# Kernel optimization log

Hardware: AMD Instinct MI355X
Metric: run time of the kernel (lower is better)

The kernel has to match this reference:

```python
import jax, jax.numpy as jnp
import numpy as np

HID = 128
NH = 4
HD = HID // NH
SCALE = HD ** -0.5
EPS = 1e-8


def setup_inputs() -> dict:
    key = jax.random.key(0)
    ks = jax.random.split(key, 10)
    C, S, H = 4, 4096, HID
    x = jax.random.normal(ks[0], (C, S, H), dtype=jnp.float32)
    edge_weight = jax.random.uniform(ks[1], (C, S, S), dtype=jnp.float32)
    def lin(kw, kb):
        W = jax.random.normal(kw, (H, H), dtype=jnp.float32) * (1.0 / np.sqrt(H))
        b = jax.random.normal(kb, (H,), dtype=jnp.float32) * 0.01
        return W, b
    Wq, bq = lin(ks[2], ks[3])
    Wk, bk = lin(ks[4], ks[5])
    Wv, bv = lin(ks[6], ks[7])
    Wo, bo = lin(ks[8], ks[9])
    return {"x": x, "edge_weight": edge_weight,
            "Wq": Wq, "bq": bq, "Wk": Wk, "bk": bk,
            "Wv": Wv, "bv": bv, "Wo": Wo, "bo": bo}


def reference(x, edge_weight, Wq, bq, Wk, bk, Wv, bv, Wo, bo):
    C, S, H = x.shape
    # projections (torch Linear: x @ W.T + b), split into heads -> (C, nh, S, hd)
    def proj(W, b):
        return (x @ W.T + b).reshape(C, S, NH, HD).transpose(0, 2, 1, 3)
    q = proj(Wq, bq)
    k = proj(Wk, bk)
    v = proj(Wv, bv)
    # scores with additive log structure bias: (C, nh, S, S)
    scores = jnp.einsum('chqd,chkd->chqk', q, k) * SCALE
    scores = scores + jnp.log(jnp.maximum(edge_weight, EPS))[:, None, :, :]
    attn = jax.nn.softmax(scores, axis=-1)  # dropout is identity in eval
    out = jnp.einsum('chqk,chkd->chqd', attn, v)
    out = out.transpose(0, 2, 1, 3).reshape(C, S, H)
    return out @ Wo.T + bo
```

## Files before the change

### kernel.cpp

```cpp
#include <hip/hip_runtime.h>
#include <hip/hip_bf16.h>
#include <cstdint>

#define S_LEN 4096
#define NHEAD 4
#define HDIM 32
#define HID 128
#define CBATCH 4
#define EPSW 1e-8f
#define NCHUNKS (S_LEN / 32)

typedef __attribute__((ext_vector_type(8))) short short8v;
typedef __attribute__((ext_vector_type(4))) float float4v;

__device__ __forceinline__ unsigned short f2bf(float f) {
    unsigned int u = __float_as_uint(f);
    return (unsigned short)((u + 0x7fffu + ((u >> 16) & 1u)) >> 16);
}

__device__ __forceinline__ float exp2_asm(float x) {
    float r;
    asm("v_exp_f32 %0, %1" : "=v"(r) : "v"(x));
    return r;
}

__device__ __forceinline__ unsigned cvt_pk_bf16(float lo, float hi) {
    unsigned r;
    asm("v_cvt_pk_bf16_f32 %0, %1, %2" : "=v"(r) : "v"(lo), "v"(hi));
    return r;
}

__device__ __forceinline__ void gload16(const void* g, void* l) {
    __builtin_amdgcn_global_load_lds(
        (const __attribute__((address_space(1))) void*)g,
        (__attribute__((address_space(3))) void*)l,
        16, 0, 0);
}

__global__ __launch_bounds__(256) void qkv_proj_kernel(
    const float* __restrict__ x,
    const float* __restrict__ Wq, const float* __restrict__ bq,
    const float* __restrict__ Wk, const float* __restrict__ bk,
    const float* __restrict__ Wv, const float* __restrict__ bv,
    unsigned short* __restrict__ Qo, unsigned short* __restrict__ Ko,
    unsigned short* __restrict__ Vo)
{
    __shared__ float xs[64][132];
    __shared__ float wsT[64][68];

    const int tid = threadIdx.x;
    const int mrow0 = blockIdx.x * 64;
    const int n0 = blockIdx.y * 64;
    const int p = blockIdx.z;
    const float* W    = (p == 0) ? Wq : (p == 1) ? Wk : Wv;
    const float* bias = (p == 0) ? bq : (p == 1) ? bk : bv;
    unsigned short* Out = (p == 0) ? Qo : (p == 1) ? Ko : Vo;

    for (int i = tid; i < 64 * 32; i += 256) {
        int r = i >> 5, c4 = (i & 31) * 4;
        *(float4*)&xs[r][c4] = *(const float4*)&x[(size_t)(mrow0 + r) * HID + c4];
    }

    float acc[4][4] = {};
    const int tr = tid >> 4;
    const int tc = tid & 15;

    for (int ph = 0; ph < 2; ++ph) {
        __syncthreads();
        for (int i = tid; i < 64 * 16; i += 256) {
            int r = i >> 4, c4 = (i & 15) * 4;
            float4 wv = *(const float4*)&W[(size_t)(n0 + r) * HID + ph * 64 + c4];
            wsT[c4 + 0][r] = wv.x;
            wsT[c4 + 1][r] = wv.y;
            wsT[c4 + 2][r] = wv.z;
            wsT[c4 + 3][r] = wv.w;
        }
        __syncthreads();
        #pragma unroll 4
        for (int k4 = 0; k4 < 16; ++k4) {
            float4 xv[4];
            #pragma unroll
            for (int i = 0; i < 4; ++i)
                xv[i] = *(const float4*)&xs[tr * 4 + i][ph * 64 + k4 * 4];
            #pragma unroll
            for (int kk = 0; kk < 4; ++kk) {
                float4 wv = *(const float4*)&wsT[k4 * 4 + kk][tc * 4];
                #pragma unroll
                for (int i = 0; i < 4; ++i) {
                    float xk = ((const float*)&xv[i])[kk];
                    acc[i][0] += xk * wv.x;
                    acc[i][1] += xk * wv.y;
                    acc[i][2] += xk * wv.z;
                    acc[i][3] += xk * wv.w;
                }
            }
        }
    }

    const float scale = (p == 0) ? 0.25500544458521289f : 1.0f;
    float4 bv4 = *(const float4*)&bias[n0 + tc * 4];
    const int nbase = n0 + tc * 4;
    const int h = nbase >> 5;
    const int d = nbase & 31;
    #pragma unroll
    for (int i = 0; i < 4; ++i) {
        int m = mrow0 + tr * 4 + i;
        int c = m >> 12, s = m & 4095;
        unsigned short pk[4];
        pk[0] = f2bf((acc[i][0] + bv4.x) * scale);
        pk[1] = f2bf((acc[i][1] + bv4.y) * scale);
        pk[2] = f2bf((acc[i][2] + bv4.z) * scale);
        pk[3] = f2bf((acc[i][3] + bv4.w) * scale);
        *(uint2*)&Out[((size_t)(c * NHEAD + h) * S_LEN + s) * HDIM + d] = *(uint2*)pk;
    }
}

__global__ __launch_bounds__(256) void vtrans_kernel(
    const unsigned short* __restrict__ V, unsigned short* __restrict__ Vt2)
{
    __shared__ unsigned short vs[64][40];
    const int tid = threadIdx.x;
    const int chh = blockIdx.y;
    const int s0 = blockIdx.x * 64;
    const size_t base = (size_t)chh * S_LEN * HDIM;
    {
        int r = tid >> 2, ch = (tid & 3) * 8;
        *(uint4*)&vs[r][ch] = *(const uint4*)&V[base + (size_t)(s0 + r) * HDIM + ch];
    }
    __syncthreads();
    {
        const int lchunk = tid >> 7;
        const int db = (tid >> 6) & 1;
        const int l = tid & 63;
        const int li = l & 15;
        const int g = l >> 4;
        unsigned short pk[8];
        #pragma unroll
        for (int j = 0; j < 8; ++j) {
            int key = lchunk * 32 + ((j < 4) ? (4 * g + j) : (16 + 4 * g + (j - 4)));
            pk[j] = vs[key][db * 16 + li];
        }
        size_t chunk = (size_t)(s0 >> 5) + lchunk;
        *(uint4*)&Vt2[(((size_t)chh * 2 + db) * NCHUNKS + chunk) * 512 + l * 8] = *(uint4*)pk;
    }
}

template<int NS>
__global__ __launch_bounds__(256) void attn_kernel(
    const unsigned short* __restrict__ Q, const unsigned short* __restrict__ K,
    const unsigned short* __restrict__ Vt2, const float* __restrict__ ew,
    unsigned short* __restrict__ partO, float* __restrict__ den)
{
    const int KCHUNK = S_LEN / NS;
    const int NIT = KCHUNK / 32;

    __shared__ float ew_lds[3][1024];

    const int tid = threadIdx.x;
    const int w = tid >> 6;
    const int lane = tid & 63;
    const int li = lane & 15;
    const int g = lane >> 4;
    const int c = blockIdx.y;
    const int qbase = blockIdx.x * 32;
    const int split = blockIdx.z;
    const int kb0 = split * KCHUNK;
    const int chh = c * NHEAD + w;

    const size_t hb = (size_t)chh * S_LEN * HDIM;
    const unsigned short* Qh = Q + hb;
    const unsigned short* Kh = K + hb;
    const float* ewc = ew + (size_t)c * S_LEN * S_LEN;

    short8v qf0 = *(const short8v*)&Qh[(size_t)(qbase + li) * HDIM + g * 8];
    short8v qf1 = *(const short8v*)&Qh[(size_t)(qbase + 16 + li) * HDIM + g * 8];

    const float* ew_src = ewc + (size_t)(qbase + (w >> 1) * 16 + li) * S_LEN + kb0
                        + (w & 1) * 16 + g * 4;
    const unsigned short* kp  = Kh + (size_t)(kb0 + li) * HDIM + g * 8;
    const unsigned short* vp0 = Vt2 + (((size_t)chh * 2 + 0) * NCHUNKS + (kb0 >> 5)) * 512 + lane * 8;
    const unsigned short* vp1 = Vt2 + (((size_t)chh * 2 + 1) * NCHUNKS + (kb0 >> 5)) * 512 + lane * 8;

    float4v o00 = {}, o01 = {}, o10 = {}, o11 = {};
    float den0 = 0.f, den1 = 0.f;
    const float4v zero4 = {0.f, 0.f, 0.f, 0.f};

    #define CFENCE() asm volatile("" ::: "memory")

    short8v kf0 = *(const short8v*)kp;
    short8v kf1 = *(const short8v*)(kp + 512);
    short8v vf0 = *(const short8v*)vp0;
    short8v vf1 = *(const short8v*)vp1;
    CFENCE();
    gload16(ew_src,      &ew_lds[0][w * 256]);
    gload16(ew_src + 32, &ew_lds[1][w * 256]);
    ew_src += 64;
    CFENCE();

    int bew = 0;
    int sew = 2;
    for (int it = 0; it < NIT; ++it) {
        if (it > 0) {
            CFENCE();
            __builtin_amdgcn_s_barrier();
        }
        short8v nkf0, nkf1, nvf0, nvf1;
        if (it + 1 < NIT) {
            nkf0 = *(const short8v*)(kp + 1024);
            nkf1 = *(const short8v*)(kp + 1536);
            nvf0 = *(const short8v*)(vp0 + 512);
            nvf1 = *(const short8v*)(vp1 + 512);
        }
        CFENCE();
        if (it + 2 < NIT) {
            gload16(ew_src, &ew_lds[sew][w * 256]);
            ew_src += 32;
        }
        if (it == 0)               asm volatile("s_waitcnt vmcnt(6)" ::: "memory");
        else if (it + 2 < NIT)     asm volatile("s_waitcnt vmcnt(10)" ::: "memory");
        else if (it + 1 < NIT)     asm volatile("s_waitcnt vmcnt(9)" ::: "memory");
        else                       asm volatile("s_waitcnt vmcnt(4)" ::: "memory");
        __builtin_amdgcn_s_barrier();
        CFENCE();

        const float* eb = ew_lds[bew];
        float4 e00 = *(const float4*)&eb[lane * 4];
        float4 e01 = *(const float4*)&eb[256 + lane * 4];
        float4 e10 = *(const float4*)&eb[512 + lane * 4];
        float4 e11 = *(const float4*)&eb[768 + lane * 4];

        float4v s0 = __builtin_amdgcn_mfma_f32_16x16x32_bf16(kf0, qf0, zero4, 0, 0, 0);
        float4v s1 = __builtin_amdgcn_mfma_f32_16x16x32_bf16(kf1, qf0, zero4, 0, 0, 0);
        float4v s2 = __builtin_amdgcn_mfma_f32_16x16x32_bf16(kf0, qf1, zero4, 0, 0, 0);
        float4v s3 = __builtin_amdgcn_mfma_f32_16x16x32_bf16(kf1, qf1, zero4, 0, 0, 0);

        float p0 = fmaxf(e00.x, EPSW) * exp2_asm(s0[0]);
        float p1 = fmaxf(e00.y, EPSW) * exp2_asm(s0[1]);
        float p2 = fmaxf(e00.z, EPSW) * exp2_asm(s0[2]);
        float p3 = fmaxf(e00.w, EPSW) * exp2_asm(s0[3]);
        float p4 = fmaxf(e01.x, EPSW) * exp2_asm(s1[0]);
        float p5 = fmaxf(e01.y, EPSW) * exp2_asm(s1[1]);
        float p6 = fmaxf(e01.z, EPSW) * exp2_asm(s1[2]);
        float p7 = fmaxf(e01.w, EPSW) * exp2_asm(s1[3]);
        union { short8v v; unsigned u[4]; } pu0;
        pu0.u[0] = cvt_pk_bf16(p0, p1);
        pu0.u[1] = cvt_pk_bf16(p2, p3);
        pu0.u[2] = cvt_pk_bf16(p4, p5);
        pu0.u[3] = cvt_pk_bf16(p6, p7);
        den0 += ((p0 + p1) + (p2 + p3)) + ((p4 + p5) + (p6 + p7));
        o00 = __builtin_amdgcn_mfma_f32_16x16x32_bf16(vf0, pu0.v, o00, 0, 0, 0);
        o01 = __builtin_amdgcn_mfma_f32_16x16x32_bf16(vf1, pu0.v, o01, 0, 0, 0);

        float r0 = fmaxf(e10.x, EPSW) * exp2_asm(s2[0]);
        float r1 = fmaxf(e10.y, EPSW) * exp2_asm(s2[1]);
        float r2 = fmaxf(e10.z, EPSW) * exp2_asm(s2[2]);
        float r3 = fmaxf(e10.w, EPSW) * exp2_asm(s2[3]);
        float r4 = fmaxf(e11.x, EPSW) * exp2_asm(s3[0]);
        float r5 = fmaxf(e11.y, EPSW) * exp2_asm(s3[1]);
        float r6 = fmaxf(e11.z, EPSW) * exp2_asm(s3[2]);
        float r7 = fmaxf(e11.w, EPSW) * exp2_asm(s3[3]);
        union { short8v v; unsigned u[4]; } pu1;
        pu1.u[0] = cvt_pk_bf16(r0, r1);
        pu1.u[1] = cvt_pk_bf16(r2, r3);
        pu1.u[2] = cvt_pk_bf16(r4, r5);
        pu1.u[3] = cvt_pk_bf16(r6, r7);
        den1 += ((r0 + r1) + (r2 + r3)) + ((r4 + r5) + (r6 + r7));
        o10 = __builtin_amdgcn_mfma_f32_16x16x32_bf16(vf0, pu1.v, o10, 0, 0, 0);
        o11 = __builtin_amdgcn_mfma_f32_16x16x32_bf16(vf1, pu1.v, o11, 0, 0, 0);

        if (it + 1 < NIT) {
            kf0 = nkf0; kf1 = nkf1; vf0 = nvf0; vf1 = nvf1;
            kp += 1024; vp0 += 512; vp1 += 512;
        }
        bew = (bew == 2) ? 0 : bew + 1;
        sew = (sew == 2) ? 0 : sew + 1;
    }
    #undef CFENCE

    den0 += __shfl_xor(den0, 16, 64);
    den0 += __shfl_xor(den0, 32, 64);
    den1 += __shfl_xor(den1, 16, 64);
    den1 += __shfl_xor(den1, 32, 64);

    const size_t pbase = (((size_t)split * CBATCH + c) * NHEAD + w) * S_LEN + qbase;
    {
        const size_t pb = pbase + li;
        uint2 s;
        s.x = cvt_pk_bf16(o00[0], o00[1]);
        s.y = cvt_pk_bf16(o00[2], o00[3]);
        *(uint2*)&partO[pb * HDIM + 0 * 16 + g * 4] = s;
        s.x = cvt_pk_bf16(o01[0], o01[1]);
        s.y = cvt_pk_bf16(o01[2], o01[3]);
        *(uint2*)&partO[pb * HDIM + 1 * 16 + g * 4] = s;
        if (g == 0) den[pb] = den0;
    }
    {
        const size_t pb = pbase + 16 + li;
        uint2 s;
        s.x = cvt_pk_bf16(o10[0], o10[1]);
        s.y = cvt_pk_bf16(o10[2], o10[3]);
        *(uint2*)&partO[pb * HDIM + 0 * 16 + g * 4] = s;
        s.x = cvt_pk_bf16(o11[0], o11[1]);
        s.y = cvt_pk_bf16(o11[2], o11[3]);
        *(uint2*)&partO[pb * HDIM + 1 * 16 + g * 4] = s;
        if (g == 0) den[pb] = den1;
    }
}

template<int NS>
__global__ __launch_bounds__(256) void combine_kernel(
    const unsigned short* __restrict__ pO, const float* __restrict__ den,
    float* __restrict__ attnbuf)
{
    const int idx = blockIdx.x * 256 + threadIdx.x;
    const int d4 = idx & 7;
    const int q  = (idx >> 3) & (S_LEN - 1);
    const int h  = (idx >> 15) & 3;
    const int c  = idx >> 17;

    const size_t bq = ((size_t)c * NHEAD + h) * S_LEN + q;
    const size_t plane = (size_t)CBATCH * NHEAD * S_LEN;
    float4 acc = {0.f, 0.f, 0.f, 0.f};
    float dsum = 0.f;
    #pragma unroll
    for (int s = 0; s < NS; ++s) {
        const size_t b = (size_t)s * plane + bq;
        uint2 a = *(const uint2*)&pO[b * HDIM + d4 * 4];
        acc.x += __uint_as_float(a.x << 16);
        acc.y += __uint_as_float(a.x & 0xffff0000u);
        acc.z += __uint_as_float(a.y << 16);
        acc.w += __uint_as_float(a.y & 0xffff0000u);
        dsum += den[b];
    }
    float inv = 1.0f / dsum;
    float4 o;
    o.x = acc.x * inv;
    o.y = acc.y * inv;
    o.z = acc.z * inv;
    o.w = acc.w * inv;
    *(float4*)&attnbuf[((size_t)c * S_LEN + q) * HID + h * HDIM + d4 * 4] = o;
}

__global__ __launch_bounds__(256) void out_proj_kernel(
    const float* __restrict__ ain, const float* __restrict__ Wo,
    const float* __restrict__ bo, float* __restrict__ out)
{
    __shared__ float xs[64][132];
    __shared__ float wsT[64][68];

    const int tid = threadIdx.x;
    const int mrow0 = blockIdx.x * 64;
    const int n0 = blockIdx.y * 64;

    for (int i = tid; i < 64 * 32; i += 256) {
        int r = i >> 5, c4 = (i & 31) * 4;
        *(float4*)&xs[r][c4] = *(const float4*)&ain[(size_t)(mrow0 + r) * HID + c4];
    }

    float acc[4][4] = {};
    const int tr = tid >> 4;
    const int tc = tid & 15;

    for (int ph = 0; ph < 2; ++ph) {
        __syncthreads();
        for (int i = tid; i < 64 * 16; i += 256) {
            int r = i >> 4, c4 = (i & 15) * 4;
            float4 wv = *(const float4*)&Wo[(size_t)(n0 + r) * HID + ph * 64 + c4];
            wsT[c4 + 0][r] = wv.x;
            wsT[c4 + 1][r] = wv.y;
            wsT[c4 + 2][r] = wv.z;
            wsT[c4 + 3][r] = wv.w;
        }
        __syncthreads();
        #pragma unroll 4
        for (int k4 = 0; k4 < 16; ++k4) {
            float4 xv[4];
            #pragma unroll
            for (int i = 0; i < 4; ++i)
                xv[i] = *(const float4*)&xs[tr * 4 + i][ph * 64 + k4 * 4];
            #pragma unroll
            for (int kk = 0; kk < 4; ++kk) {
                float4 wv = *(const float4*)&wsT[k4 * 4 + kk][tc * 4];
                #pragma unroll
                for (int i = 0; i < 4; ++i) {
                    float xk = ((const float*)&xv[i])[kk];
                    acc[i][0] += xk * wv.x;
                    acc[i][1] += xk * wv.y;
                    acc[i][2] += xk * wv.z;
                    acc[i][3] += xk * wv.w;
                }
            }
        }
    }

    float4 bv4 = *(const float4*)&bo[n0 + tc * 4];
    #pragma unroll
    for (int i = 0; i < 4; ++i) {
        int m = mrow0 + tr * 4 + i;
        float4 o;
        o.x = acc[i][0] + bv4.x;
        o.y = acc[i][1] + bv4.y;
        o.z = acc[i][2] + bv4.z;
        o.w = acc[i][3] + bv4.w;
        *(float4*)&out[(size_t)m * HID + n0 + tc * 4] = o;
    }
}

extern "C" void kernel_launch(void* const* d_in, const int* in_sizes, int n_in,
                              void* d_out, int out_size, void* d_ws, size_t ws_size,
                              hipStream_t stream) {
    const float* x  = (const float*)d_in[0];
    const float* ew = (const float*)d_in[1];
    const float* Wq = (const float*)d_in[2];
    const float* bq = (const float*)d_in[3];
    const float* Wk = (const float*)d_in[4];
    const float* bk = (const float*)d_in[5];
    const float* Wv = (const float*)d_in[6];
    const float* bv = (const float*)d_in[7];
    const float* Wo = (const float*)d_in[8];
    const float* bo = (const float*)d_in[9];
    float* out = (float*)d_out;

    char* ws = (char*)d_ws;
    const size_t QSZ = (size_t)CBATCH * NHEAD * S_LEN * HDIM * sizeof(unsigned short);
    const size_t PLANE_O16 = (size_t)CBATCH * NHEAD * S_LEN * HDIM * sizeof(unsigned short);
    const size_t PLANE_D = (size_t)CBATCH * NHEAD * S_LEN * sizeof(float);

    const size_t need4 = 3 * QSZ + 4 * PLANE_O16 + 4 * PLANE_D;
    const int ns = (ws_size >= need4) ? 4 : 2;

    unsigned short* Qw  = (unsigned short*)(ws);
    unsigned short* Kw  = (unsigned short*)(ws + QSZ);
    unsigned short* Vt2 = (unsigned short*)(ws + 2 * QSZ);
    unsigned short* Vw  = (unsigned short*)(ws + 3 * QSZ);
    unsigned short* partO = (unsigned short*)(ws + 3 * QSZ);
    float* den   = (float*)(ws + 3 * QSZ + (size_t)ns * PLANE_O16);
    float* attnbuf = (float*)(ws);

    qkv_proj_kernel<<<dim3(256, 2, 3), 256, 0, stream>>>(x, Wq, bq, Wk, bk, Wv, bv, Qw, Kw, Vw);
    vtrans_kernel<<<dim3(S_LEN / 64, CBATCH * NHEAD), 256, 0, stream>>>(Vw, Vt2);
    if (ns == 4) {
        attn_kernel<4><<<dim3(S_LEN / 32, CBATCH, 4), 256, 0, stream>>>(Qw, Kw, Vt2, ew, partO, den);
        combine_kernel<4><<<dim3((CBATCH * S_LEN * HID / 4) / 256), 256, 0, stream>>>(partO, den, attnbuf);
    } else {
        attn_kernel<2><<<dim3(S_LEN / 32, CBATCH, 2), 256, 0, stream>>>(Qw, Kw, Vt2, ew, partO, den);
        combine_kernel<2><<<dim3((CBATCH * S_LEN * HID / 4) / 256), 256, 0, stream>>>(partO, den, attnbuf);
    }
    out_proj_kernel<<<dim3(256, 2), 256, 0, stream>>>(attnbuf, Wo, bo, out);
}
```

Baseline: 174.4 us.

## Process 64 keys per attention iteration with one barrier per step

The attention main loop now handles two 32-key sub-tiles per iteration, so the iteration count is halved. Each iteration stages a 2048-float edge-weight tile in a triple-buffered LDS ring with a prefetch distance of one, and drops the extra leading barrier. K/V fragments for both sub-tiles are loaded at the top of the same iteration instead of being prefetched into registers one iteration ahead. The aim is to cut barrier and loop overhead and give more independent MFMA/exp work per step. The cost is that K/V load latency may be less hidden, and LDS use doubles to 24 KB per block, which could lower occupancy.

```diff
diff --git a/kernel.cpp b/kernel.cpp
--- a/kernel.cpp
+++ b/kernel.cpp
@@ -152,9 +152,9 @@
     unsigned short* __restrict__ partO, float* __restrict__ den)
 {
     const int KCHUNK = S_LEN / NS;
-    const int NIT = KCHUNK / 32;
-
-    __shared__ float ew_lds[3][1024];
+    const int NIT = KCHUNK / 64;
+
+    __shared__ float ew_lds[3][2048];
 
     const int tid = threadIdx.x;
     const int w = tid >> 6;
@@ -175,8 +175,9 @@
     short8v qf0 = *(const short8v*)&Qh[(size_t)(qbase + li) * HDIM + g * 8];
     short8v qf1 = *(const short8v*)&Qh[(size_t)(qbase + 16 + li) * HDIM + g * 8];
 
-    const float* ew_src = ewc + (size_t)(qbase + (w >> 1) * 16 + li) * S_LEN + kb0
-                        + (w & 1) * 16 + g * 4;
+    const float* ewA_src = ewc + (size_t)(qbase + (w >> 1) * 16 + li) * S_LEN + kb0
+                         + (w & 1) * 16 + g * 4;
+    const float* ewB_src = ewA_src + 32;
     const unsigned short* kp  = Kh + (size_t)(kb0 + li) * HDIM + g * 8;
     const unsigned short* vp0 = Vt2 + (((size_t)chh * 2 + 0) * NCHUNKS + (kb0 >> 5)) * 512 + lane * 8;
     const unsigned short* vp1 = Vt2 + (((size_t)chh * 2 + 1) * NCHUNKS + (kb0 >> 5)) * 512 + lane * 8;
@@ -187,91 +188,130 @@
 
     #define CFENCE() asm volatile("" ::: "memory")
 
-    short8v kf0 = *(const short8v*)kp;
-    short8v kf1 = *(const short8v*)(kp + 512);
-    short8v vf0 = *(const short8v*)vp0;
-    short8v vf1 = *(const short8v*)vp1;
+    gload16(ewA_src, &ew_lds[0][w * 256]);
+    gload16(ewB_src, &ew_lds[0][1024 + w * 256]);
+    ewA_src += 64; ewB_src += 64;
     CFENCE();
-    gload16(ew_src,      &ew_lds[0][w * 256]);
-    gload16(ew_src + 32, &ew_lds[1][w * 256]);
-    ew_src += 64;
-    CFENCE();
 
     int bew = 0;
-    int sew = 2;
+    int sew = 1;
     for (int it = 0; it < NIT; ++it) {
-        if (it > 0) {
-            CFENCE();
-            __builtin_amdgcn_s_barrier();
-        }
-        short8v nkf0, nkf1, nvf0, nvf1;
+        short8v kfA0 = *(const short8v*)kp;
+        short8v kfA1 = *(const short8v*)(kp + 512);
+        short8v vfA0 = *(const short8v*)vp0;
+        short8v vfA1 = *(const short8v*)vp1;
+        short8v kfB0 = *(const short8v*)(kp + 1024);
+        short8v kfB1 = *(const short8v*)(kp + 1536);
+        short8v vfB0 = *(const short8v*)(vp0 + 512);
+        short8v vfB1 = *(const short8v*)(vp1 + 512);
+        CFENCE();
         if (it + 1 < NIT) {
-            nkf0 = *(const short8v*)(kp + 1024);
-            nkf1 = *(const short8v*)(kp + 1536);
-            nvf0 = *(const short8v*)(vp0 + 512);
-            nvf1 = *(const short8v*)(vp1 + 512);
-        }
-        CFENCE();
-        if (it + 2 < NIT) {
-            gload16(ew_src, &ew_lds[sew][w * 256]);
-            ew_src += 32;
-        }
-        if (it == 0)               asm volatile("s_waitcnt vmcnt(6)" ::: "memory");
-        else if (it + 2 < NIT)     asm volatile("s_waitcnt vmcnt(10)" ::: "memory");
-        else if (it + 1 < NIT)     asm volatile("s_waitcnt vmcnt(9)" ::: "memory");
-        else                       asm volatile("s_waitcnt vmcnt(4)" ::: "memory");
+            gload16(ewA_src, &ew_lds[sew][w * 256]);
+            gload16(ewB_src, &ew_lds[sew][1024 + w * 256]);
+            ewA_src += 64; ewB_src += 64;
+        }
+        if (it + 1 < NIT) asm volatile("s_waitcnt vmcnt(10)" ::: "memory");
+        else              asm volatile("s_waitcnt vmcnt(8)" ::: "memory");
         __builtin_amdgcn_s_barrier();
         CFENCE();
 
         const float* eb = ew_lds[bew];
-        float4 e00 = *(const float4*)&eb[lane * 4];
-        float4 e01 = *(const float4*)&eb[256 + lane * 4];
-        float4 e10 = *(const float4*)&eb[512 + lane * 4];
-        float4 e11 = *(const float4*)&eb[768 + lane * 4];
-
-        float4v s0 = __builtin_amdgcn_mfma_f32_16x16x32_bf16(kf0, qf0, zero4, 0, 0, 0);
-        float4v s1 = __builtin_amdgcn_mfma_f32_16x16x32_bf16(kf1, qf0, zero4, 0, 0, 0);
-        float4v s2 = __builtin_amdgcn_mfma_f32_16x16x32_bf16(kf0, qf1, zero4, 0, 0, 0);
-        float4v s3 = __builtin_amdgcn_mfma_f32_16x16x32_bf16(kf1, qf1, zero4, 0, 0, 0);
-
-        float p0 = fmaxf(e00.x, EPSW) * exp2_asm(s0[0]);
-        float p1 = fmaxf(e00.y, EPSW) * exp2_asm(s0[1]);
-        float p2 = fmaxf(e00.z, EPSW) * exp2_asm(s0[2]);
-        float p3 = fmaxf(e00.w, EPSW) * exp2_asm(s0[3]);
-        float p4 = fmaxf(e01.x, EPSW) * exp2_asm(s1[0]);
-        float p5 = fmaxf(e01.y, EPSW) * exp2_asm(s1[1]);
-        float p6 = fmaxf(e01.z, EPSW) * exp2_asm(s1[2]);
-        float p7 = fmaxf(e01.w, EPSW) * exp2_asm(s1[3]);
-        union { short8v v; unsigned u[4]; } pu0;
-        pu0.u[0] = cvt_pk_bf16(p0, p1);
-        pu0.u[1] = cvt_pk_bf16(p2, p3);
-        pu0.u[2] = cvt_pk_bf16(p4, p5);
-        pu0.u[3] = cvt_pk_bf16(p6, p7);
-        den0 += ((p0 + p1) + (p2 + p3)) + ((p4 + p5) + (p6 + p7));
-        o00 = __builtin_amdgcn_mfma_f32_16x16x32_bf16(vf0, pu0.v, o00, 0, 0, 0);
-        o01 = __builtin_amdgcn_mfma_f32_16x16x32_bf16(vf1, pu0.v, o01, 0, 0, 0);
-
-        float r0 = fmaxf(e10.x, EPSW) * exp2_asm(s2[0]);
-        float r1 = fmaxf(e10.y, EPSW) * exp2_asm(s2[1]);
-        float r2 = fmaxf(e10.z, EPSW) * exp2_asm(s2[2]);
-        float r3 = fmaxf(e10.w, EPSW) * exp2_asm(s2[3]);
-        float r4 = fmaxf(e11.x, EPSW) * exp2_asm(s3[0]);
-        float r5 = fmaxf(e11.y, EPSW) * exp2_asm(s3[1]);
-        float r6 = fmaxf(e11.z, EPSW) * exp2_asm(s3[2]);
-        float r7 = fmaxf(e11.w, EPSW) * exp2_asm(s3[3]);
-        union { short8v v; unsigned u[4]; } pu1;
-        pu1.u[0] = cvt_pk_bf16(r0, r1);
-        pu1.u[1] = cvt_pk_bf16(r2, r3);
-        pu1.u[2] = cvt_pk_bf16(r4, r5);
-        pu1.u[3] = cvt_pk_bf16(r6, r7);
-        den1 += ((r0 + r1) + (r2 + r3)) + ((r4 + r5) + (r6 + r7));
-        o10 = __builtin_amdgcn_mfma_f32_16x16x32_bf16(vf0, pu1.v, o10, 0, 0, 0);
-        o11 = __builtin_amdgcn_mfma_f32_16x16x32_bf16(vf1, pu1.v, o11, 0, 0, 0);
-
-        if (it + 1 < NIT) {
-            kf0 = nkf0; kf1 = nkf1; vf0 = nvf0; vf1 = nvf1;
-            kp += 1024; vp0 += 512; vp1 += 512;
-        }
+
+        {
+            float4 e00 = *(const float4*)&eb[lane * 4];
+            float4 e01 = *(const float4*)&eb[256 + lane * 4];
+            float4 e10 = *(const float4*)&eb[512 + lane * 4];
+            float4 e11 = *(const float4*)&eb[768 + lane * 4];
+
+            float4v s0 = __builtin_amdgcn_mfma_f32_16x16x32_bf16(kfA0, qf0, zero4, 0, 0, 0);
+            float4v s1 = __builtin_amdgcn_mfma_f32_16x16x32_bf16(kfA1, qf0, zero4, 0, 0, 0);
+            float4v s2 = __builtin_amdgcn_mfma_f32_16x16x32_bf16(kfA0, qf1, zero4, 0, 0, 0);
+            float4v s3 = __builtin_amdgcn_mfma_f32_16x16x32_bf16(kfA1, qf1, zero4, 0, 0, 0);
+
+            float p0 = fmaxf(e00.x, EPSW) * exp2_asm(s0[0]);
+            float p1 = fmaxf(e00.y, EPSW) * exp2_asm(s0[1]);
+            float p2 = fmaxf(e00.z, EPSW) * exp2_asm(s0[2]);
+            float p3 = fmaxf(e00.w, EPSW) * exp2_asm(s0[3]);
+            float p4 = fmaxf(e01.x, EPSW) * exp2_asm(s1[0]);
+            float p5 = fmaxf(e01.y, EPSW) * exp2_asm(s1[1]);
+            float p6 = fmaxf(e01.z, EPSW) * exp2_asm(s1[2]);
+            float p7 = fmaxf(e01.w, EPSW) * exp2_asm(s1[3]);
+            union { short8v v; unsigned u[4]; } pu0;
+            pu0.u[0] = cvt_pk_bf16(p0, p1);
+            pu0.u[1] = cvt_pk_bf16(p2, p3);
+            pu0.u[2] = cvt_pk_bf16(p4, p5);
+            pu0.u[3] = cvt_pk_bf16(p6, p7);
+            den0 += ((p0 + p1) + (p2 + p3)) + ((p4 + p5) + (p6 + p7));
+            o00 = __builtin_amdgcn_mfma_f32_16x16x32_bf16(vfA0, pu0.v, o00, 0, 0, 0);
+            o01 = __builtin_amdgcn_mfma_f32_16x16x32_bf16(vfA1, pu0.v, o01, 0, 0, 0);
+
+            float r0 = fmaxf(e10.x, EPSW) * exp2_asm(s2[0]);
+            float r1 = fmaxf(e10.y, EPSW) * exp2_asm(s2[1]);
+            float r2 = fmaxf(e10.z, EPSW) * exp2_asm(s2[2]);
+            float r3 = fmaxf(e10.w, EPSW) * exp2_asm(s2[3]);
+            float r4 = fmaxf(e11.x, EPSW) * exp2_asm(s3[0]);
+            float r5 = fmaxf(e11.y, EPSW) * exp2_asm(s3[1]);
+            float r6 = fmaxf(e11.z, EPSW) * exp2_asm(s3[2]);
+            float r7 = fmaxf(e11.w, EPSW) * exp2_asm(s3[3]);
+            union { short8v v; unsigned u[4]; } pu1;
+            pu1.u[0] = cvt_pk_bf16(r0, r1);
+            pu1.u[1] = cvt_pk_bf16(r2, r3);
+            pu1.u[2] = cvt_pk_bf16(r4, r5);
+            pu1.u[3] = cvt_pk_bf16(r6, r7);
+            den1 += ((r0 + r1) + (r2 + r3)) + ((r4 + r5) + (r6 + r7));
+            o10 = __builtin_amdgcn_mfma_f32_16x16x32_bf16(vfA0, pu1.v, o10, 0, 0, 0);
+            o11 = __builtin_amdgcn_mfma_f32_16x16x32_bf16(vfA1, pu1.v, o11, 0, 0, 0);
+        }
+
+        {
+            float4 e00 = *(const float4*)&eb[1024 + lane * 4];
+            float4 e01 = *(const float4*)&eb[1280 + lane * 4];
+            float4 e10 = *(const float4*)&eb[1536 + lane * 4];
+            float4 e11 = *(const float4*)&eb[1792 + lane * 4];
+
+            float4v s0 = __builtin_amdgcn_mfma_f32_16x16x32_bf16(kfB0, qf0, zero4, 0, 0, 0);
+            float4v s1 = __builtin_amdgcn_mfma_f32_16x16x32_bf16(kfB1, qf0, zero4, 0, 0, 0);
+            float4v s2 = __builtin_amdgcn_mfma_f32_16x16x32_bf16(kfB0, qf1, zero4, 0, 0, 0);
+            float4v s3 = __builtin_amdgcn_mfma_f32_16x16x32_bf16(kfB1, qf1, zero4, 0, 0, 0);
+
+            float p0 = fmaxf(e00.x, EPSW) * exp2_asm(s0[0]);
+            float p1 = fmaxf(e00.y, EPSW) * exp2_asm(s0[1]);
+            float p2 = fmaxf(e00.z, EPSW) * exp2_asm(s0[2]);
+            float p3 = fmaxf(e00.w, EPSW) * exp2_asm(s0[3]);
+            float p4 = fmaxf(e01.x, EPSW) * exp2_asm(s1[0]);
+            float p5 = fmaxf(e01.y, EPSW) * exp2_asm(s1[1]);
+            float p6 = fmaxf(e01.z, EPSW) * exp2_asm(s1[2]);
+            float p7 = fmaxf(e01.w, EPSW) * exp2_asm(s1[3]);
+            union { short8v v; unsigned u[4]; } pu0;
+            pu0.u[0] = cvt_pk_bf16(p0, p1);
+            pu0.u[1] = cvt_pk_bf16(p2, p3);
+            pu0.u[2] = cvt_pk_bf16(p4, p5);
+            pu0.u[3] = cvt_pk_bf16(p6, p7);
+            den0 += ((p0 + p1) + (p2 + p3)) + ((p4 + p5) + (p6 + p7));
+            o00 = __builtin_amdgcn_mfma_f32_16x16x32_bf16(vfB0, pu0.v, o00, 0, 0, 0);
+            o01 = __builtin_amdgcn_mfma_f32_16x16x32_bf16(vfB1, pu0.v, o01, 0, 0, 0);
+
+            float r0 = fmaxf(e10.x, EPSW) * exp2_asm(s2[0]);
+            float r1 = fmaxf(e10.y, EPSW) * exp2_asm(s2[1]);
+            float r2 = fmaxf(e10.z, EPSW) * exp2_asm(s2[2]);
+            float r3 = fmaxf(e10.w, EPSW) * exp2_asm(s2[3]);
+            float r4 = fmaxf(e11.x, EPSW) * exp2_asm(s3[0]);
+            float r5 = fmaxf(e11.y, EPSW) * exp2_asm(s3[1]);
+            float r6 = fmaxf(e11.z, EPSW) * exp2_asm(s3[2]);
+            float r7 = fmaxf(e11.w, EPSW) * exp2_asm(s3[3]);
+            union { short8v v; unsigned u[4]; } pu1;
+            pu1.u[0] = cvt_pk_bf16(r0, r1);
+            pu1.u[1] = cvt_pk_bf16(r2, r3);
+            pu1.u[2] = cvt_pk_bf16(r4, r5);
+            pu1.u[3] = cvt_pk_bf16(r6, r7);
+            den1 += ((r0 + r1) + (r2 + r3)) + ((r4 + r5) + (r6 + r7));
+            o10 = __builtin_amdgcn_mfma_f32_16x16x32_bf16(vfB0, pu1.v, o10, 0, 0, 0);
+            o11 = __builtin_amdgcn_mfma_f32_16x16x32_bf16(vfB1, pu1.v, o11, 0, 0, 0);
+        }
+
+        kp += 2048;
+        vp0 += 1024;
+        vp1 += 1024;
         bew = (bew == 2) ? 0 : bew + 1;
         sew = (sew == 2) ? 0 : sew + 1;
     }
```

Measured after the change: 169.9 us. -2.6%, faster.
